# Performance work log

Hardware: AMD Instinct MI355X
Metric: run time of the kernel (lower is better)

The kernel has to match this reference:

```python
import jax, jax.numpy as jnp
import numpy as np

EMBED = 512
HEADS = 8
HEAD_DIM = EMBED // HEADS


def setup_inputs() -> dict:
    key = jax.random.key(0)
    ks = jax.random.split(key, 9)
    B, P, S, E = 32, 512, 1024, EMBED
    query = jax.random.normal(ks[0], (B, P, E), dtype=jnp.float32)
    k_in = jax.random.normal(ks[1], (B, S, E), dtype=jnp.float32)
    v_in = jax.random.normal(ks[2], (B, S, E), dtype=jnp.float32)
    key_padding_mask = jax.random.randint(ks[3], (B, P, S), 0, 2).astype(bool)
    sc = 1.0 / np.sqrt(E)
    Wq = jax.random.normal(ks[4], (E, E), dtype=jnp.float32) * sc
    Wk = jax.random.normal(ks[5], (E, E), dtype=jnp.float32) * sc
    Wv = jax.random.normal(ks[6], (E, E), dtype=jnp.float32) * sc
    Wo = jax.random.normal(ks[7], (E, E), dtype=jnp.float32) * sc
    bo = jax.random.normal(ks[8], (E,), dtype=jnp.float32) * 0.01
    return {"query": query, "key": k_in, "value": v_in,
            "key_padding_mask": key_padding_mask,
            "Wq": Wq, "Wk": Wk, "Wv": Wv, "Wo": Wo, "bo": bo}


def reference(query, key, value, key_padding_mask, Wq, Wk, Wv, Wo, bo):
    B, P, E = query.shape
    S = key.shape[1]
    H, D = HEADS, HEAD_DIM
    scale = D ** -0.5
    # Linear projections (torch Linear: x @ W.T)
    Q = (query @ Wq.T).reshape(B, P, H, D).transpose(0, 2, 1, 3)  # [B,H,P,D]
    K = (key @ Wk.T).reshape(B, S, H, D).transpose(0, 2, 1, 3)    # [B,H,S,D]
    V = (value @ Wv.T).reshape(B, S, H, D).transpose(0, 2, 1, 3)  # [B,H,S,D]
    scores = jnp.einsum('bhpd,bhsd->bhps', Q, K) * scale          # [B,H,P,S]
    mask = key_padding_mask[:, None, :, :]                        # [B,1,P,S]
    scores = jnp.where(mask, -jnp.inf, scores)
    attn = jax.nn.softmax(scores, axis=-1)
    ctx = jnp.einsum('bhps,bhsd->bhpd', attn, V)                  # [B,H,P,D]
    ctx = ctx.transpose(0, 2, 1, 3).reshape(B, P, E)
    return ctx @ Wo.T + bo
```

## Files before the change

### kernel.cpp

```cpp
#include <hip/hip_runtime.h>

#define B_  32
#define P_  512
#define S_  1024
#define E_  512
#define H_  8
#define D_  64

typedef unsigned int uint32;
typedef unsigned short u16;
typedef __attribute__((ext_vector_type(8))) _Float16 half8;
typedef __attribute__((ext_vector_type(4))) float f32x4;

__device__ __forceinline__ u16 f2h_bits(float f){
  _Float16 h = (_Float16)f;
  union { _Float16 h; u16 u; } cv; cv.h = h; return cv.u;
}
__device__ __forceinline__ half8 cvt8(f32x4 a, f32x4 b){
  half8 h;
  h[0]=(_Float16)a[0]; h[1]=(_Float16)a[1]; h[2]=(_Float16)a[2]; h[3]=(_Float16)a[3];
  h[4]=(_Float16)b[0]; h[5]=(_Float16)b[1]; h[6]=(_Float16)b[2]; h[7]=(_Float16)b[3];
  return h;
}
__device__ __forceinline__ f32x4 mfma16(half8 a, half8 b, f32x4 c){
  return __builtin_amdgcn_mfma_f32_16x16x32_f16(a, b, c, 0, 0, 0);
}
#define GLD16(ldsp, gp) __builtin_amdgcn_global_load_lds( \
    (const __attribute__((address_space(1))) void*)(gp), \
    (__attribute__((address_space(3))) void*)(ldsp), 16, 0, 0)

__global__ void cvt_w_kernel(const float* __restrict__ w0, const float* __restrict__ w1,
                             const float* __restrict__ w2, u16* __restrict__ out){
  int i = blockIdx.x * 256 + threadIdx.x;
  int region = i >> 15;
  int off = (i & 32767) * 8;
  const float* s = (region == 0) ? w0 : (region == 1) ? w1 : w2;
  f32x4 a = *(const f32x4*)(s + off);
  f32x4 b = *(const f32x4*)(s + off + 4);
  *(half8*)(out + region * 262144 + off) = cvt8(a, b);
}

__global__ void detect_mask_kernel(const uint32* __restrict__ m, int* __restrict__ flag){
  __shared__ int s_gt1, s_bgt1;
  if (threadIdx.x == 0){ s_gt1 = 0; s_bgt1 = 0; }
  __syncthreads();
  int gt1 = 0, bgt1 = 0;
  for (int i = threadIdx.x; i < 4096; i += 256){
    uint32 w = m[i];
    if (w > 1u) gt1 = 1;
    if (((w)&0xffu) > 1u || ((w>>8)&0xffu) > 1u || ((w>>16)&0xffu) > 1u || ((w>>24)&0xffu) > 1u) bgt1 = 1;
  }
  if (gt1)  atomicOr(&s_gt1, 1);
  if (bgt1) atomicOr(&s_bgt1, 1);
  __syncthreads();
  if (threadIdx.x == 0) *flag = s_gt1 ? (s_bgt1 ? 2 : 1) : 0;
}

__global__ void pack_mask_kernel(const uint32* __restrict__ m, const int* __restrict__ flag,
                                 uint32* __restrict__ bits){
  const int w = blockIdx.x * 256 + threadIdx.x;
  const int f = *flag;
  uint32 out = 0u;
  if (f == 1){
    #pragma unroll
    for (int i = 0; i < 8; i++){
      uint32 v = m[(size_t)w*8 + i];
      if (v & 0x000000ffu) out |= 1u << (i*4 + 0);
      if (v & 0x0000ff00u) out |= 1u << (i*4 + 1);
      if (v & 0x00ff0000u) out |= 1u << (i*4 + 2);
      if (v & 0xff000000u) out |= 1u << (i*4 + 3);
    }
  } else {
    #pragma unroll
    for (int i = 0; i < 32; i++){
      if (m[(size_t)w*32 + i]) out |= 1u << i;
    }
  }
  bits[w] = out;
}

template<int MODE, int A16, int B16, int SWZ>
__global__ __launch_bounds__(256) void gemm_f(
    const void* __restrict__ Ap, const void* __restrict__ Bp,
    void* __restrict__ Cp, const float* __restrict__ bias, int rshift)
{
  __shared__ __align__(16) u16 As[128*64];
  __shared__ __align__(16) u16 Bs[128*64];
  const int tid  = threadIdx.x;
  const int lane = tid & 63;
  const int wv   = tid >> 6;
  const int lrow = lane & 15, khi = lane >> 4;
  const int wm   = wv >> 1,  wn  = wv & 1;

  int bx = blockIdx.x, by = blockIdx.y;
  if (SWZ){
    const int nbx = gridDim.x;
    const int nwg = nbx * gridDim.y;
    const int bid = by * nbx + bx;
    const int l = (bid & 7) * (nwg >> 3) + (bid >> 3);
    by = l / nbx; bx = l - by * nbx;
  }
  const long gm0 = (long)by * 128;
  const long gn0 = (long)bx * 128;

  f32x4 acc[4][4];
  #pragma unroll
  for (int i = 0; i < 4; i++)
    #pragma unroll
    for (int j = 0; j < 4; j++) acc[i][j] = (f32x4){0.f,0.f,0.f,0.f};

  #pragma unroll 1
  for (int kk = 0; kk < 512; kk += 64){
    if (kk) __syncthreads();
    if (A16){
      const u16* ab = (const u16*)Ap;
      #pragma unroll
      for (int j = 0; j < 4; j++){
        int row = j*32 + (tid >> 3);
        GLD16(&As[j*2048 + tid*8], ab + (gm0 + row)*512 + kk + (tid & 7)*8);
      }
    } else {
      const float* ap = (const float*)Ap + (gm0 + (tid>>1))*512 + kk + (tid&1)*32;
      const int lidx = (tid>>1)*64 + (tid&1)*32;
      #pragma unroll
      for (int i = 0; i < 4; i++){
        f32x4 f0 = *(const f32x4*)(ap + i*8);
        f32x4 f1 = *(const f32x4*)(ap + i*8 + 4);
        *(half8*)&As[lidx + i*8] = cvt8(f0, f1);
      }
    }
    if (B16){
      const u16* bb = (const u16*)Bp;
      #pragma unroll
      for (int j = 0; j < 4; j++){
        int row = j*32 + (tid >> 3);
        GLD16(&Bs[j*2048 + tid*8], bb + (gn0 + row)*512 + kk + (tid & 7)*8);
      }
    } else {
      const float* bp = (const float*)Bp + (gn0 + (tid>>1))*512 + kk + (tid&1)*32;
      const int lidx = (tid>>1)*64 + (tid&1)*32;
      #pragma unroll
      for (int i = 0; i < 4; i++){
        f32x4 f0 = *(const f32x4*)(bp + i*8);
        f32x4 f1 = *(const f32x4*)(bp + i*8 + 4);
        *(half8*)&Bs[lidx + i*8] = cvt8(f0, f1);
      }
    }
    __syncthreads();

    half8 af[4][2], bf[4][2];
    #pragma unroll
    for (int mi = 0; mi < 4; mi++){
      const u16* p = &As[(wm*64 + mi*16 + lrow)*64 + khi*8];
      af[mi][0] = *(const half8*)p;
      af[mi][1] = *(const half8*)(p + 32);
    }
    #pragma unroll
    for (int ni = 0; ni < 4; ni++){
      const u16* p = &Bs[(wn*64 + ni*16 + lrow)*64 + khi*8];
      bf[ni][0] = *(const half8*)p;
      bf[ni][1] = *(const half8*)(p + 32);
    }
    #pragma unroll
    for (int mi = 0; mi < 4; mi++)
      #pragma unroll
      for (int ni = 0; ni < 4; ni++){
        acc[mi][ni] = mfma16(af[mi][0], bf[ni][0], acc[mi][ni]);
        acc[mi][ni] = mfma16(af[mi][1], bf[ni][1], acc[mi][ni]);
      }
  }

  #pragma unroll
  for (int mi = 0; mi < 4; mi++)
    #pragma unroll
    for (int ni = 0; ni < 4; ni++)
      #pragma unroll
      for (int r = 0; r < 4; r++){
        long gm = gm0 + wm*64 + mi*16 + khi*4 + r;
        long gn = gn0 + wn*64 + ni*16 + lrow;
        float v = acc[mi][ni][r];
        if (MODE == 0){
          long b  = gm >> rshift;
          long rr = gm & ((1L << rshift) - 1);
          long h  = gn >> 6, d = gn & 63;
          ((u16*)Cp)[((b*8 + h) << (rshift + 6)) + rr*64 + d] = f2h_bits(v);
        } else if (MODE == 1){
          long b = gn >> 10, s = gn & 1023;
          ((u16*)Cp)[b*524288 + gm*1024 + s] = f2h_bits(v);
        } else {
          ((float*)Cp)[gm*512 + gn] = v + bias[gn];
        }
      }
}

__device__ __forceinline__ int swz(int row, int col){ return row*64 + (col ^ ((row & 7) << 3)); }

__global__ __launch_bounds__(256) void attn_kernel(
    const u16* __restrict__ Qb, const u16* __restrict__ Kb,
    const u16* __restrict__ Vtb, const uint32* __restrict__ bits,
    u16* __restrict__ Ctx)
{
  __shared__ __align__(16) u16 Ks[64*64];
  __shared__ __align__(16) u16 Vs[64*64];
  __shared__ __align__(16) u16 Ps[64*64];
  __shared__ uint32 mlds[64][2];

  const int tid  = threadIdx.x;
  const int lane = tid & 63;
  const int wv   = tid >> 6;
  const int lrow = lane & 15, khi = lane >> 4;

  const int bidx = blockIdx.x;
  const int logical = (bidx & 7) * 256 + (bidx >> 3);
  const int bh = logical >> 3;
  const int p0 = (logical & 7) * 64;
  const int bb = bh >> 3;

  const u16* qp = Qb  + (size_t)bh * (P_*64) + (size_t)p0 * 64;
  const u16* kp = Kb  + (size_t)bh * (S_*64);
  const u16* vp = Vtb + (size_t)bh * (D_*S_);

  {
    int row = tid >> 2, cb = (tid & 3) * 16;
    const u16* src = qp + (size_t)row*64 + cb;
    *(half8*)&Ps[swz(row, cb)]     = *(const half8*)src;
    *(half8*)&Ps[swz(row, cb + 8)] = *(const half8*)(src + 8);
  }
  __syncthreads();
  half8 aq0, aq1;
  {
    const int row = wv*16 + lrow;
    aq0 = *(const half8*)&Ps[swz(row, khi*8)];
    aq1 = *(const half8*)&Ps[swz(row, khi*8 + 32)];
  }

  f32x4 accO[4];
  #pragma unroll
  for (int i = 0; i < 4; i++) accO[i] = (f32x4){0.f,0.f,0.f,0.f};
  float mst[4], lst[4];
  #pragma unroll
  for (int r = 0; r < 4; r++){ mst[r] = -1e30f; lst[r] = 0.f; }

  const float SCL = 0.125f * 1.44269504f;

  #pragma unroll 1
  for (int s0 = 0; s0 < S_; s0 += 64){
    __syncthreads();
    {
      int row = tid >> 2, cb = (tid & 3) * 16;
      const u16* ksrc = kp + (size_t)(s0 + row)*64 + cb;
      *(half8*)&Ks[swz(row, cb)]     = *(const half8*)ksrc;
      *(half8*)&Ks[swz(row, cb + 8)] = *(const half8*)(ksrc + 8);
      const u16* vsrc = vp + (size_t)row*S_ + s0 + cb;
      *(half8*)&Vs[swz(row, cb)]     = *(const half8*)vsrc;
      *(half8*)&Vs[swz(row, cb + 8)] = *(const half8*)(vsrc + 8);
    }
    if (tid < 128){
      int row = tid >> 1, wsel = tid & 1;
      mlds[row][wsel] = bits[(size_t)(bb*P_ + p0 + row)*(S_/32) + (s0 >> 5) + wsel];
    }
    __syncthreads();

    f32x4 sc[4];
    #pragma unroll
    for (int ssub = 0; ssub < 4; ssub++){
      const int r_ = ssub*16 + lrow;
      half8 bk0 = *(const half8*)&Ks[swz(r_, khi*8)];
      half8 bk1 = *(const half8*)&Ks[swz(r_, khi*8 + 32)];
      f32x4 c = (f32x4){0.f,0.f,0.f,0.f};
      c = mfma16(aq0, bk0, c);
      c = mfma16(aq1, bk1, c);
      sc[ssub] = c;
    }

    float fac[4];
    #pragma unroll
    for (int r = 0; r < 4; r++){
      const int prow = wv*16 + khi*4 + r;
      const uint32 mw0 = mlds[prow][0];
      const uint32 mw1 = mlds[prow][1];
      #pragma unroll
      for (int ssub = 0; ssub < 4; ssub++){
        int sloc = ssub*16 + lrow;
        uint32 mw = (ssub < 2) ? mw0 : mw1;
        float v = sc[ssub][r] * SCL;
        if ((mw >> (sloc & 31)) & 1u) v = -1e30f;
        sc[ssub][r] = v;
      }
      float mx = fmaxf(fmaxf(sc[0][r], sc[1][r]), fmaxf(sc[2][r], sc[3][r]));
      #pragma unroll
      for (int off = 1; off < 16; off <<= 1) mx = fmaxf(mx, __shfl_xor(mx, off));
      float mnew = fmaxf(mst[r], mx);
      fac[r] = __builtin_amdgcn_exp2f(mst[r] - mnew);
      float ts = 0.f;
      #pragma unroll
      for (int ssub = 0; ssub < 4; ssub++){
        float pv = __builtin_amdgcn_exp2f(sc[ssub][r] - mnew);
        sc[ssub][r] = pv;
        ts += pv;
      }
      #pragma unroll
      for (int off = 1; off < 16; off <<= 1) ts += __shfl_xor(ts, off);
      lst[r] = lst[r]*fac[r] + ts;
      mst[r] = mnew;
    }
    #pragma unroll
    for (int dsub = 0; dsub < 4; dsub++){
      f32x4 a = accO[dsub];
      a[0] *= fac[0]; a[1] *= fac[1]; a[2] *= fac[2]; a[3] *= fac[3];
      accO[dsub] = a;
    }

    #pragma unroll
    for (int ssub = 0; ssub < 4; ssub++)
      #pragma unroll
      for (int r = 0; r < 4; r++)
        Ps[swz(wv*16 + khi*4 + r, ssub*16 + lrow)] = f2h_bits(sc[ssub][r]);
    __syncthreads();

    half8 ap0, ap1;
    {
      const int row = wv*16 + lrow;
      ap0 = *(const half8*)&Ps[swz(row, khi*8)];
      ap1 = *(const half8*)&Ps[swz(row, khi*8 + 32)];
    }
    #pragma unroll
    for (int dsub = 0; dsub < 4; dsub++){
      const int r_ = dsub*16 + lrow;
      half8 bv0 = *(const half8*)&Vs[swz(r_, khi*8)];
      half8 bv1 = *(const half8*)&Vs[swz(r_, khi*8 + 32)];
      accO[dsub] = mfma16(ap0, bv0, accO[dsub]);
      accO[dsub] = mfma16(ap1, bv1, accO[dsub]);
    }
  }

  const int hh = bh & 7;
  #pragma unroll
  for (int r = 0; r < 4; r++){
    float inv = __builtin_amdgcn_rcpf(lst[r]);
    #pragma unroll
    for (int dsub = 0; dsub < 4; dsub++){
      int prow = p0 + wv*16 + khi*4 + r;
      float v = accO[dsub][r] * inv;
      Ctx[(size_t)(bb*P_ + prow)*E_ + hh*64 + dsub*16 + lrow] = f2h_bits(v);
    }
  }
}

extern "C" void kernel_launch(void* const* d_in, const int* in_sizes, int n_in,
                              void* d_out, int out_size, void* d_ws, size_t ws_size,
                              hipStream_t stream)
{
  const float* query = (const float*)d_in[0];
  const float* key   = (const float*)d_in[1];
  const float* value = (const float*)d_in[2];
  const void*  mask  = d_in[3];
  const float* Wq = (const float*)d_in[4];
  const float* Wk = (const float*)d_in[5];
  const float* Wv = (const float*)d_in[6];
  const float* Wo = (const float*)d_in[7];
  const float* bo = (const float*)d_in[8];

  char* ws = (char*)d_ws;
  u16*    Qb   = (u16*)(ws);
  u16*    Kb   = (u16*)(ws + (16u  << 20));
  u16*    Vtb  = (u16*)(ws + (48u  << 20));
  u16*    Ctx  = (u16*)(ws + (80u  << 20));
  uint32* bits = (uint32*)(ws + (96u << 20));
  int*    flag = (int*)(ws + (98u << 20));
  u16*    WqkvH= Ctx;

  cvt_w_kernel<<<384, 256, 0, stream>>>(Wq, Wk, Wv, WqkvH);
  detect_mask_kernel<<<1, 256, 0, stream>>>((const uint32*)mask, flag);
  pack_mask_kernel<<<2048, 256, 0, stream>>>((const uint32*)mask, flag, bits);
  gemm_f<0,0,1,1><<<dim3(4, 128), 256, 0, stream>>>((const void*)query, (const void*)(WqkvH),
                                                    (void*)Qb, nullptr, 9);
  gemm_f<0,0,1,1><<<dim3(4, 256), 256, 0, stream>>>((const void*)key, (const void*)(WqkvH + 262144),
                                                    (void*)Kb, nullptr, 10);
  gemm_f<1,1,0,0><<<dim3(256, 4), 256, 0, stream>>>((const void*)(WqkvH + 524288), (const void*)value,
                                                    (void*)Vtb, nullptr, 0);
  attn_kernel<<<2048, 256, 0, stream>>>(Qb, Kb, Vtb, bits, Ctx);
  gemm_f<2,1,0,1><<<dim3(4, 128), 256, 0, stream>>>((const void*)Ctx, (const void*)Wo,
                                                    d_out, bo, 0);
}
```

Before: 480.8 us.

## Transpose attention MFMA to keep P in registers, pre-convert K/V/Wo to fp16

The attention kernel now computes S^T = K·Q^T so each lane holds a full query row. That makes the softmax row reductions mostly lane-local, and the probability tile is rearranged with ds_bpermute instead of an LDS round trip and an extra barrier. The P LDS buffer is removed, and output stores are packed into 8-byte writes. Separately, key, value and Wo are converted to fp16 up front so the K/V/out projections read half-precision inputs. This adds a full conversion pass over K and V, and workspace buffers are aliased, including mask bits stored temporarily in the output buffer.

```diff
diff --git a/kernel.cpp b/kernel.cpp
--- a/kernel.cpp
+++ b/kernel.cpp
@@ -10,11 +10,18 @@
 typedef unsigned int uint32;
 typedef unsigned short u16;
 typedef __attribute__((ext_vector_type(8))) _Float16 half8;
+typedef __attribute__((ext_vector_type(2))) __fp16 fp16x2;
 typedef __attribute__((ext_vector_type(4))) float f32x4;
+typedef __attribute__((ext_vector_type(2))) uint32 u32x2;
 
 __device__ __forceinline__ u16 f2h_bits(float f){
   _Float16 h = (_Float16)f;
   union { _Float16 h; u16 u; } cv; cv.h = h; return cv.u;
+}
+__device__ __forceinline__ uint32 pk16(float a, float b){
+  union { fp16x2 h; uint32 u; } cv;
+  cv.h = __builtin_amdgcn_cvt_pkrtz(a, b);
+  return cv.u;
 }
 __device__ __forceinline__ half8 cvt8(f32x4 a, f32x4 b){
   half8 h;
@@ -29,12 +36,25 @@
     (const __attribute__((address_space(1))) void*)(gp), \
     (__attribute__((address_space(3))) void*)(ldsp), 16, 0, 0)
 
+__global__ void cvt_kv_kernel(const float* __restrict__ key, const float* __restrict__ value,
+                              u16* __restrict__ Kh, u16* __restrict__ Vh){
+  size_t i = (size_t)blockIdx.x * 256 + threadIdx.x;
+  int region = (int)(i >> 21);
+  size_t off = (i & 2097151) * 8;
+  const float* s = region ? value : key;
+  u16* d = region ? Vh : Kh;
+  f32x4 a = *(const f32x4*)(s + off);
+  f32x4 b = *(const f32x4*)(s + off + 4);
+  *(half8*)(d + off) = cvt8(a, b);
+}
+
 __global__ void cvt_w_kernel(const float* __restrict__ w0, const float* __restrict__ w1,
-                             const float* __restrict__ w2, u16* __restrict__ out){
+                             const float* __restrict__ w2, const float* __restrict__ w3,
+                             u16* __restrict__ out){
   int i = blockIdx.x * 256 + threadIdx.x;
   int region = i >> 15;
   int off = (i & 32767) * 8;
-  const float* s = (region == 0) ? w0 : (region == 1) ? w1 : w2;
+  const float* s = (region == 0) ? w0 : (region == 1) ? w1 : (region == 2) ? w2 : w3;
   f32x4 a = *(const f32x4*)(s + off);
   f32x4 b = *(const f32x4*)(s + off + 4);
   *(half8*)(out + region * 262144 + off) = cvt8(a, b);
@@ -202,7 +222,6 @@
 {
   __shared__ __align__(16) u16 Ks[64*64];
   __shared__ __align__(16) u16 Vs[64*64];
-  __shared__ __align__(16) u16 Ps[64*64];
   __shared__ uint32 mlds[64][2];
 
   const int tid  = threadIdx.x;
@@ -223,25 +242,26 @@
   {
     int row = tid >> 2, cb = (tid & 3) * 16;
     const u16* src = qp + (size_t)row*64 + cb;
-    *(half8*)&Ps[swz(row, cb)]     = *(const half8*)src;
-    *(half8*)&Ps[swz(row, cb + 8)] = *(const half8*)(src + 8);
+    *(half8*)&Ks[swz(row, cb)]     = *(const half8*)src;
+    *(half8*)&Ks[swz(row, cb + 8)] = *(const half8*)(src + 8);
   }
   __syncthreads();
-  half8 aq0, aq1;
+  half8 q_lo, q_hi;
   {
     const int row = wv*16 + lrow;
-    aq0 = *(const half8*)&Ps[swz(row, khi*8)];
-    aq1 = *(const half8*)&Ps[swz(row, khi*8 + 32)];
+    q_lo = *(const half8*)&Ks[swz(row, khi*8)];
+    q_hi = *(const half8*)&Ks[swz(row, khi*8 + 32)];
   }
 
   f32x4 accO[4];
   #pragma unroll
   for (int i = 0; i < 4; i++) accO[i] = (f32x4){0.f,0.f,0.f,0.f};
-  float mst[4], lst[4];
-  #pragma unroll
-  for (int r = 0; r < 4; r++){ mst[r] = -1e30f; lst[r] = 0.f; }
+  float mst = -1e30f, lst = 0.f;
 
   const float SCL = 0.125f * 1.44269504f;
+  const int srcA = (lrow + 16*((2*khi)    & 3)) << 2;
+  const int srcB = (lrow + 16*((2*khi + 1)& 3)) << 2;
+  const bool hiH = khi >= 2;
 
   #pragma unroll 1
   for (int s0 = 0; s0 < S_; s0 += 64){
@@ -264,86 +284,106 @@
     f32x4 sc[4];
     #pragma unroll
     for (int ssub = 0; ssub < 4; ssub++){
-      const int r_ = ssub*16 + lrow;
-      half8 bk0 = *(const half8*)&Ks[swz(r_, khi*8)];
-      half8 bk1 = *(const half8*)&Ks[swz(r_, khi*8 + 32)];
+      const int rr = ssub*16 + lrow;
+      half8 k_lo = *(const half8*)&Ks[swz(rr, khi*8)];
+      half8 k_hi = *(const half8*)&Ks[swz(rr, khi*8 + 32)];
       f32x4 c = (f32x4){0.f,0.f,0.f,0.f};
-      c = mfma16(aq0, bk0, c);
-      c = mfma16(aq1, bk1, c);
+      c = mfma16(k_lo, q_lo, c);
+      c = mfma16(k_hi, q_hi, c);
       sc[ssub] = c;
     }
 
-    float fac[4];
-    #pragma unroll
-    for (int r = 0; r < 4; r++){
-      const int prow = wv*16 + khi*4 + r;
-      const uint32 mw0 = mlds[prow][0];
-      const uint32 mw1 = mlds[prow][1];
-      #pragma unroll
-      for (int ssub = 0; ssub < 4; ssub++){
-        int sloc = ssub*16 + lrow;
-        uint32 mw = (ssub < 2) ? mw0 : mw1;
+    const uint32 mw0 = mlds[wv*16 + lrow][0];
+    const uint32 mw1 = mlds[wv*16 + lrow][1];
+    float mx = -1e30f;
+    #pragma unroll
+    for (int ssub = 0; ssub < 4; ssub++){
+      const uint32 mw = (ssub < 2) ? mw0 : mw1;
+      #pragma unroll
+      for (int r = 0; r < 4; r++){
+        const int s = ssub*16 + khi*4 + r;
         float v = sc[ssub][r] * SCL;
-        if ((mw >> (sloc & 31)) & 1u) v = -1e30f;
+        if ((mw >> (s & 31)) & 1u) v = -1e30f;
         sc[ssub][r] = v;
-      }
-      float mx = fmaxf(fmaxf(sc[0][r], sc[1][r]), fmaxf(sc[2][r], sc[3][r]));
-      #pragma unroll
-      for (int off = 1; off < 16; off <<= 1) mx = fmaxf(mx, __shfl_xor(mx, off));
-      float mnew = fmaxf(mst[r], mx);
-      fac[r] = __builtin_amdgcn_exp2f(mst[r] - mnew);
-      float ts = 0.f;
-      #pragma unroll
-      for (int ssub = 0; ssub < 4; ssub++){
-        float pv = __builtin_amdgcn_exp2f(sc[ssub][r] - mnew);
-        sc[ssub][r] = pv;
-        ts += pv;
-      }
-      #pragma unroll
-      for (int off = 1; off < 16; off <<= 1) ts += __shfl_xor(ts, off);
-      lst[r] = lst[r]*fac[r] + ts;
-      mst[r] = mnew;
-    }
+        mx = fmaxf(mx, v);
+      }
+    }
+    mx = fmaxf(mx, __shfl_xor(mx, 16));
+    mx = fmaxf(mx, __shfl_xor(mx, 32));
+    const float mnew = fmaxf(mst, mx);
+    const float fac = __builtin_amdgcn_exp2f(mst - mnew);
+    float ts = 0.f;
+    #pragma unroll
+    for (int ssub = 0; ssub < 4; ssub++)
+      #pragma unroll
+      for (int r = 0; r < 4; r++){
+        float p = __builtin_amdgcn_exp2f(sc[ssub][r] - mnew);
+        sc[ssub][r] = p;
+        ts += p;
+      }
+    ts += __shfl_xor(ts, 16);
+    ts += __shfl_xor(ts, 32);
+    lst = lst * fac + ts;
+    mst = mnew;
+    #pragma unroll
+    for (int d = 0; d < 4; d++){
+      f32x4 a = accO[d];
+      a[0] *= fac; a[1] *= fac; a[2] *= fac; a[3] *= fac;
+      accO[d] = a;
+    }
+
+    uint32 w00 = pk16(sc[0][0], sc[0][1]), w01 = pk16(sc[0][2], sc[0][3]);
+    uint32 w10 = pk16(sc[1][0], sc[1][1]), w11 = pk16(sc[1][2], sc[1][3]);
+    uint32 w20 = pk16(sc[2][0], sc[2][1]), w21 = pk16(sc[2][2], sc[2][3]);
+    uint32 w30 = pk16(sc[3][0], sc[3][1]), w31 = pk16(sc[3][2], sc[3][3]);
+
+    union { half8 h; uint32 u[4]; } plo, phi;
+    {
+      uint32 t0 = __builtin_amdgcn_ds_bpermute(srcA, (int)w00);
+      uint32 t1 = __builtin_amdgcn_ds_bpermute(srcA, (int)w10);
+      plo.u[0] = hiH ? t1 : t0;
+      t0 = __builtin_amdgcn_ds_bpermute(srcA, (int)w01);
+      t1 = __builtin_amdgcn_ds_bpermute(srcA, (int)w11);
+      plo.u[1] = hiH ? t1 : t0;
+      t0 = __builtin_amdgcn_ds_bpermute(srcB, (int)w00);
+      t1 = __builtin_amdgcn_ds_bpermute(srcB, (int)w10);
+      plo.u[2] = hiH ? t1 : t0;
+      t0 = __builtin_amdgcn_ds_bpermute(srcB, (int)w01);
+      t1 = __builtin_amdgcn_ds_bpermute(srcB, (int)w11);
+      plo.u[3] = hiH ? t1 : t0;
+      t0 = __builtin_amdgcn_ds_bpermute(srcA, (int)w20);
+      t1 = __builtin_amdgcn_ds_bpermute(srcA, (int)w30);
+      phi.u[0] = hiH ? t1 : t0;
+      t0 = __builtin_amdgcn_ds_bpermute(srcA, (int)w21);
+      t1 = __builtin_amdgcn_ds_bpermute(srcA, (int)w31);
+      phi.u[1] = hiH ? t1 : t0;
+      t0 = __builtin_amdgcn_ds_bpermute(srcB, (int)w20);
+      t1 = __builtin_amdgcn_ds_bpermute(srcB, (int)w30);
+      phi.u[2] = hiH ? t1 : t0;
+      t0 = __builtin_amdgcn_ds_bpermute(srcB, (int)w21);
+      t1 = __builtin_amdgcn_ds_bpermute(srcB, (int)w31);
+      phi.u[3] = hiH ? t1 : t0;
+    }
+
     #pragma unroll
     for (int dsub = 0; dsub < 4; dsub++){
-      f32x4 a = accO[dsub];
-      a[0] *= fac[0]; a[1] *= fac[1]; a[2] *= fac[2]; a[3] *= fac[3];
-      accO[dsub] = a;
-    }
-
-    #pragma unroll
-    for (int ssub = 0; ssub < 4; ssub++)
-      #pragma unroll
-      for (int r = 0; r < 4; r++)
-        Ps[swz(wv*16 + khi*4 + r, ssub*16 + lrow)] = f2h_bits(sc[ssub][r]);
-    __syncthreads();
-
-    half8 ap0, ap1;
-    {
-      const int row = wv*16 + lrow;
-      ap0 = *(const half8*)&Ps[swz(row, khi*8)];
-      ap1 = *(const half8*)&Ps[swz(row, khi*8 + 32)];
-    }
-    #pragma unroll
-    for (int dsub = 0; dsub < 4; dsub++){
-      const int r_ = dsub*16 + lrow;
-      half8 bv0 = *(const half8*)&Vs[swz(r_, khi*8)];
-      half8 bv1 = *(const half8*)&Vs[swz(r_, khi*8 + 32)];
-      accO[dsub] = mfma16(ap0, bv0, accO[dsub]);
-      accO[dsub] = mfma16(ap1, bv1, accO[dsub]);
+      const int rr = dsub*16 + lrow;
+      half8 v_lo = *(const half8*)&Vs[swz(rr, khi*8)];
+      half8 v_hi = *(const half8*)&Vs[swz(rr, khi*8 + 32)];
+      accO[dsub] = mfma16(v_lo, plo.h, accO[dsub]);
+      accO[dsub] = mfma16(v_hi, phi.h, accO[dsub]);
     }
   }
 
   const int hh = bh & 7;
+  const float inv = __builtin_amdgcn_rcpf(lst);
+  const size_t base = (size_t)(bb*P_ + p0 + wv*16 + lrow) * E_ + hh*64 + khi*4;
   #pragma unroll
-  for (int r = 0; r < 4; r++){
-    float inv = __builtin_amdgcn_rcpf(lst[r]);
-    #pragma unroll
-    for (int dsub = 0; dsub < 4; dsub++){
-      int prow = p0 + wv*16 + khi*4 + r;
-      float v = accO[dsub][r] * inv;
-      Ctx[(size_t)(bb*P_ + prow)*E_ + hh*64 + dsub*16 + lrow] = f2h_bits(v);
-    }
+  for (int dsub = 0; dsub < 4; dsub++){
+    u32x2 pkd;
+    pkd.x = pk16(accO[dsub][0] * inv, accO[dsub][1] * inv);
+    pkd.y = pk16(accO[dsub][2] * inv, accO[dsub][3] * inv);
+    *(u32x2*)&Ctx[base + dsub*16] = pkd;
   }
 }
 
@@ -362,24 +402,27 @@
   const float* bo = (const float*)d_in[8];
 
   char* ws = (char*)d_ws;
+  u16*    Vh   = (u16*)(ws);
+  u16*    Kh   = (u16*)(ws + (32u << 20));
+  u16*    Kb   = (u16*)(ws + (64u << 20));
+  u16*    Vtb  = (u16*)(ws + (32u << 20));
   u16*    Qb   = (u16*)(ws);
-  u16*    Kb   = (u16*)(ws + (16u  << 20));
-  u16*    Vtb  = (u16*)(ws + (48u  << 20));
-  u16*    Ctx  = (u16*)(ws + (80u  << 20));
-  uint32* bits = (uint32*)(ws + (96u << 20));
-  int*    flag = (int*)(ws + (98u << 20));
-  u16*    WqkvH= Ctx;
-
-  cvt_w_kernel<<<384, 256, 0, stream>>>(Wq, Wk, Wv, WqkvH);
+  u16*    Ctx  = (u16*)(ws + (16u << 20));
+  u16*    W4h  = (u16*)(ws + (96u << 20));
+  uint32* bits = (uint32*)d_out;
+  int*    flag = (int*)((char*)d_out + (2u << 20));
+
+  cvt_kv_kernel<<<16384, 256, 0, stream>>>(key, value, Kh, Vh);
+  cvt_w_kernel<<<512, 256, 0, stream>>>(Wq, Wk, Wv, Wo, W4h);
   detect_mask_kernel<<<1, 256, 0, stream>>>((const uint32*)mask, flag);
   pack_mask_kernel<<<2048, 256, 0, stream>>>((const uint32*)mask, flag, bits);
-  gemm_f<0,0,1,1><<<dim3(4, 128), 256, 0, stream>>>((const void*)query, (const void*)(WqkvH),
+  gemm_f<0,1,1,1><<<dim3(4, 256), 256, 0, stream>>>((const void*)Kh, (const void*)(W4h + 262144),
+                                                    (void*)Kb, nullptr, 10);
+  gemm_f<1,1,1,0><<<dim3(256, 4), 256, 0, stream>>>((const void*)(W4h + 524288), (const void*)Vh,
+                                                    (void*)Vtb, nullptr, 0);
+  gemm_f<0,0,1,1><<<dim3(4, 128), 256, 0, stream>>>((const void*)query, (const void*)W4h,
                                                     (void*)Qb, nullptr, 9);
-  gemm_f<0,0,1,1><<<dim3(4, 256), 256, 0, stream>>>((const void*)key, (const void*)(WqkvH + 262144),
-                                                    (void*)Kb, nullptr, 10);
-  gemm_f<1,1,0,0><<<dim3(256, 4), 256, 0, stream>>>((const void*)(WqkvH + 524288), (const void*)value,
-                                                    (void*)Vtb, nullptr, 0);
   attn_kernel<<<2048, 256, 0, stream>>>(Qb, Kb, Vtb, bits, Ctx);
-  gemm_f<2,1,0,1><<<dim3(4, 128), 256, 0, stream>>>((const void*)Ctx, (const void*)Wo,
+  gemm_f<2,1,1,1><<<dim3(4, 128), 256, 0, stream>>>((const void*)Ctx, (const void*)(W4h + 786432),
                                                     d_out, bo, 0);
 }
```

Result: faster. 430.9 us (-10.4%).
